# Optimization experiments

Measured on AMD Instinct MI355X. Metric: run time of the kernel, lower is better.

## Reference

```python
import jax, jax.numpy as jnp
import numpy as np

C_S, C_Z, H, P_QK, P_V, L = 384, 128, 12, 4, 8, 768
D = C_S // H
OUT_DIM = C_S + H * P_V * 3 + H * C_Z


def setup_inputs() -> dict:
    key = jax.random.key(0)
    ks = jax.random.split(key, 16)
    sc = lambda fan_in: 1.0 / np.sqrt(fan_in)
    inp = {
        'single': jax.random.normal(ks[0], (L, C_S), jnp.float32),
        'pair': jax.random.normal(ks[1], (L, L, C_Z), jnp.float32),
        'rots': jax.random.normal(ks[2], (L, 3, 3), jnp.float32),
        'trans': jax.random.normal(ks[3], (L, 3), jnp.float32),
        'ln_g': jnp.ones((C_S,), jnp.float32),
        'ln_b': jnp.zeros((C_S,), jnp.float32),
        'Wq': jax.random.normal(ks[4], (C_S, C_S), jnp.float32) * sc(C_S),
        'Wk': jax.random.normal(ks[5], (C_S, C_S), jnp.float32) * sc(C_S),
        'Wv': jax.random.normal(ks[6], (C_S, C_S), jnp.float32) * sc(C_S),
        'Wqp': jax.random.normal(ks[7], (C_S, H * P_QK * 3), jnp.float32) * sc(C_S),
        'bqp': jnp.zeros((H * P_QK * 3,), jnp.float32),
        'Wkp': jax.random.normal(ks[8], (C_S, H * P_QK * 3), jnp.float32) * sc(C_S),
        'bkp': jnp.zeros((H * P_QK * 3,), jnp.float32),
        'Wvp': jax.random.normal(ks[9], (C_S, H * P_V * 3), jnp.float32) * sc(C_S),
        'bvp': jnp.zeros((H * P_V * 3,), jnp.float32),
        'Wpb': jax.random.normal(ks[10], (C_Z, H), jnp.float32) * sc(C_Z),
        'head_weights': jnp.zeros((H,), jnp.float32),
        'Wo': jax.random.normal(ks[11], (OUT_DIM, C_S), jnp.float32) * sc(OUT_DIM),
        'bo': jnp.zeros((C_S,), jnp.float32),
    }
    return inp


def _layernorm(x, g, b, eps=1e-5):
    mu = x.mean(-1, keepdims=True)
    var = ((x - mu) ** 2).mean(-1, keepdims=True)
    return (x - mu) * jax.lax.rsqrt(var + eps) * g + b


def _apply_frames(pts, rots, trans):
    # pts: [L,H,P,3]; rotate each local point into global frame, then translate
    return jnp.einsum('lij,lhpj->lhpi', rots, pts) + trans[:, None, None, :]


def reference(single, pair, rots, trans, ln_g, ln_b, Wq, Wk, Wv, Wqp, bqp,
              Wkp, bkp, Wvp, bvp, Wpb, head_weights, Wo, bo):
    s = _layernorm(single, ln_g, ln_b)
    q = (s @ Wq).reshape(L, H, D)
    k = (s @ Wk).reshape(L, H, D)
    v = (s @ Wv).reshape(L, H, D)
    q_pts = (s @ Wqp + bqp).reshape(L, H, P_QK, 3)
    k_pts = (s @ Wkp + bkp).reshape(L, H, P_QK, 3)
    v_pts = (s @ Wvp + bvp).reshape(L, H, P_V, 3)

    q_g = _apply_frames(q_pts, rots, trans)
    k_g = _apply_frames(k_pts, rots, trans)
    v_g = _apply_frames(v_pts, rots, trans)

    # scalar attention logits [H, L, L]
    attn = jnp.einsum('ihd,jhd->hij', q, k) / np.sqrt(D).astype(np.float32)
    # point-distance bias: ||q_g_i - k_g_j||^2 summed over points -> [L,L,H]
    pt_diff = q_g[:, None] - k_g[None, :]            # [L,L,H,P,3]
    pt_dist_sq = (pt_diff ** 2).sum((-1, -2))        # [L,L,H]
    w_c = jax.nn.softplus(head_weights)
    attn = attn - 0.5 * w_c[:, None, None] * jnp.transpose(pt_dist_sq, (2, 0, 1))
    attn = attn + jnp.einsum('ijc,ch->hij', pair, Wpb)
    attn = jax.nn.softmax(attn, axis=-1)

    out_scalar = jnp.einsum('hij,jhd->ihd', attn, v).reshape(L, C_S)
    out_pts_g = jnp.einsum('hij,jhpc->ihpc', attn, v_g)  # [L,H,Pv,3]
    flat_pts = out_pts_g.reshape(L, H * P_V, 3) - trans[:, None, :]
    # inverse rotation = transpose: einsum with swapped rot indices
    out_pts_l = jnp.einsum('lji,lnj->lni', rots, flat_pts).reshape(L, H * P_V * 3)
    out_pair = jnp.einsum('hij,ijc->ihc', attn, pair).reshape(L, H * C_Z)

    cat = jnp.concatenate([out_scalar, out_pts_l, out_pair], axis=-1)
    return cat @ Wo + bo
```

## Files before the change

kernel.cpp:

```cpp
#include <hip/hip_runtime.h>
#include <math.h>

#define LSEQ 768
#define CS   384
#define CZ   128
#define NH   12
#define OUTD 2208
#define PROJW 1728
#define LL2  (LSEQ*LSEQ)

__device__ __forceinline__ float waveSum(float v){
#pragma unroll
  for (int o = 32; o > 0; o >>= 1) v += __shfl_down(v, o, 64);
  return v;
}

__global__ __launch_bounds__(128) void k_lnwcat(
    const float* __restrict__ x, const float* __restrict__ g,
    const float* __restrict__ b, float* __restrict__ s,
    const float* __restrict__ Wq, const float* __restrict__ Wk,
    const float* __restrict__ Wv, const float* __restrict__ Wqp,
    const float* __restrict__ Wkp, const float* __restrict__ Wvp,
    const float* __restrict__ bqp, const float* __restrict__ bkp,
    const float* __restrict__ bvp,
    float* __restrict__ wcat, float* __restrict__ bcat){
  int blk = blockIdx.x, t = threadIdx.x;
  if (blk < LSEQ){
    int i = blk;
    const float* row = x + (size_t)i*CS;
    float v0 = row[t], v1 = row[t+128], v2 = row[t+256];
    float sum = v0+v1+v2;
    float sq  = v0*v0+v1*v1+v2*v2;
    float ws1 = waveSum(sum), ws2 = waveSum(sq);
    __shared__ float red[4];
    int w = t>>6, lane = t&63;
    if (lane == 0){ red[w] = ws1; red[w+2] = ws2; }
    __syncthreads();
    float mu   = (red[0]+red[1]) * (1.f/CS);
    float var  = (red[2]+red[3]) * (1.f/CS) - mu*mu;
    float rstd = rsqrtf(var + 1e-5f);
    float* o = s + (size_t)i*CS;
    o[t]     = (v0-mu)*rstd*g[t]     + b[t];
    o[t+128] = (v1-mu)*rstd*g[t+128] + b[t+128];
    o[t+256] = (v2-mu)*rstd*g[t+256] + b[t+256];
    return;
  }
  int idx = (blk - LSEQ)*128 + t;
  if (idx < PROJW){
    float bv = 0.f;
    if (idx >= 1440)      bv = bvp[idx-1440];
    else if (idx >= 1296) bv = bkp[idx-1296];
    else if (idx >= 1152) bv = bqp[idx-1152];
    bcat[idx] = bv;
  }
  if (idx >= 384*PROJW) return;
  int r = idx / PROJW, c = idx % PROJW;
  float v;
  if (c < 384)       v = Wq[r*384 + c];
  else if (c < 768)  v = Wk[r*384 + c-384];
  else if (c < 1152) v = Wv[r*384 + c-768];
  else if (c < 1296) v = Wqp[r*144 + c-1152];
  else if (c < 1440) v = Wkp[r*144 + c-1296];
  else               v = Wvp[r*288 + c-1440];
  wcat[idx] = v;
}

__global__ __launch_bounds__(256) void k_gemm(
    const float* __restrict__ A, const float* __restrict__ B,
    const float* __restrict__ bias, float* __restrict__ C,
    int M, int N, int K, int kChunk){
  __shared__ float As[16][68];
  __shared__ float Bs[16][68];
  int j0 = blockIdx.x*64, i0 = blockIdx.y*64;
  int kBeg = blockIdx.z * kChunk;
  int t = threadIdx.x, tx = t & 15, ty = t >> 4;
  int arow = t >> 2, ak = (t & 3) * 4;
  int brow = t >> 4, bcol = (t & 15) * 4;
  float acc[4][4] = {};
  for (int kb = kBeg; kb < kBeg + kChunk; kb += 16){
    float4 av = *(const float4*)(A + (size_t)(i0+arow)*K + kb + ak);
    As[ak+0][arow]=av.x; As[ak+1][arow]=av.y; As[ak+2][arow]=av.z; As[ak+3][arow]=av.w;
    float4 bv = make_float4(0.f,0.f,0.f,0.f);
    if (j0 + bcol < N) bv = *(const float4*)(B + (size_t)(kb+brow)*N + j0 + bcol);
    *(float4*)(&Bs[brow][bcol]) = bv;
    __syncthreads();
#pragma unroll
    for (int kk = 0; kk < 16; ++kk){
      float a[4], b[4];
      *(float4*)a = *(const float4*)(&As[kk][ty*4]);
      *(float4*)b = *(const float4*)(&Bs[kk][tx*4]);
#pragma unroll
      for (int r = 0; r < 4; ++r)
#pragma unroll
        for (int c = 0; c < 4; ++c) acc[r][c] += a[r]*b[c];
    }
    __syncthreads();
  }
  bool noSplit = (gridDim.z == 1);
#pragma unroll
  for (int r = 0; r < 4; ++r){
    int i = i0 + ty*4 + r;
#pragma unroll
    for (int c = 0; c < 4; ++c){
      int j = j0 + tx*4 + c;
      if (j < N){
        float v = acc[r][c];
        if (noSplit && bias) v += bias[j];
        C[(size_t)i*N + j] = v;
      }
    }
  }
}

__global__ __launch_bounds__(256) void k_gemmWo(
    const float* __restrict__ A, const float* __restrict__ B, float* __restrict__ C){
  __shared__ float As[8][132];
  __shared__ float Bs[8][132];
  const int j0 = blockIdx.x*128, i0 = blockIdx.y*128;
  const int kBeg = blockIdx.z*184;
  const int t = threadIdx.x;
  const int arow = t >> 1, akq = (t & 1)*4;
  const int bk = t >> 5, bn = (t & 31)*4;
  const int tx = t & 15, ty = t >> 4;
  float acc[8][8] = {};
  for (int kb = kBeg; kb < kBeg+184; kb += 8){
    float4 av = *(const float4*)(A + (size_t)(i0+arow)*OUTD + kb + akq);
    float4 bv = *(const float4*)(B + (size_t)(kb+bk)*CS + j0 + bn);
    As[akq+0][arow]=av.x; As[akq+1][arow]=av.y; As[akq+2][arow]=av.z; As[akq+3][arow]=av.w;
    *(float4*)(&Bs[bk][bn]) = bv;
    __syncthreads();
#pragma unroll
    for (int k = 0; k < 8; ++k){
      float a[8], b[8];
      *(float4*)(a)   = *(const float4*)(&As[k][ty*8]);
      *(float4*)(a+4) = *(const float4*)(&As[k][ty*8+4]);
      *(float4*)(b)   = *(const float4*)(&Bs[k][tx*8]);
      *(float4*)(b+4) = *(const float4*)(&Bs[k][tx*8+4]);
#pragma unroll
      for (int r = 0; r < 8; ++r)
#pragma unroll
        for (int c = 0; c < 8; ++c) acc[r][c] += a[r]*b[c];
    }
    __syncthreads();
  }
  float* out = C + (size_t)blockIdx.z*LSEQ*CS;
#pragma unroll
  for (int r = 0; r < 8; ++r){
    float* o = out + (size_t)(i0+ty*8+r)*CS + j0 + tx*8;
    *(float4*)(o)   = make_float4(acc[r][0],acc[r][1],acc[r][2],acc[r][3]);
    *(float4*)(o+4) = make_float4(acc[r][4],acc[r][5],acc[r][6],acc[r][7]);
  }
}

__global__ __launch_bounds__(256) void k_prep(
    float* __restrict__ proj, const float* __restrict__ rots,
    const float* __restrict__ trans, const float* __restrict__ hw,
    float* __restrict__ Qa, float* __restrict__ Ka, float* __restrict__ nrm){
  int i = blockIdx.x, t = threadIdx.x;
  __shared__ float wcl[12];
  __shared__ float qg[144], kg[144];
  if (t < 12) wcl[t] = log1pf(__expf(hw[t]));
  float* prow = proj + (size_t)i*PROJW;
  if (t < 192){
    const float* R  = rots + i*9;
    const float* tr = trans + i*3;
    int off = (t < 48) ? (1152 + t*3) : ((t < 96) ? (1296 + (t-48)*3) : (1440 + (t-96)*3));
    float x = prow[off], y = prow[off+1], z = prow[off+2];
    float gx = R[0]*x + R[1]*y + R[2]*z + tr[0];
    float gy = R[3]*x + R[4]*y + R[5]*z + tr[1];
    float gz = R[6]*x + R[7]*y + R[8]*z + tr[2];
    if (t < 48){ qg[t*3]=gx; qg[t*3+1]=gy; qg[t*3+2]=gz; }
    else if (t < 96){ int u=t-48; kg[u*3]=gx; kg[u*3+1]=gy; kg[u*3+2]=gz; }
    else { prow[off]=gx; prow[off+1]=gy; prow[off+2]=gz; }
  }
  __syncthreads();
  const float isq = 0.17677669529663687f;
  for (int idx = t; idx < 576; idx += 256){
    int h = idx/48, d = idx%48;
    float qv = 0.f, kv = 0.f;
    if (d < 32){ qv = prow[h*32 + d]*isq; kv = prow[384 + h*32 + d]; }
    else if (d < 44){ qv = qg[h*12 + (d-32)]*wcl[h]; kv = kg[h*12 + (d-32)]; }
    Qa[((size_t)h*LSEQ + i)*48 + d] = qv;
    Ka[((size_t)h*LSEQ + i)*48 + d] = kv;
  }
  if (t < 24){
    int h = t % 12; int isK = (t >= 12) ? 1 : 0;
    const float* g = isK ? kg : qg;
    float sum = 0.f;
#pragma unroll
    for (int d = 0; d < 12; ++d){ float v = g[h*12+d]; sum += v*v; }
    nrm[((size_t)(isK*12 + h))*LSEQ + i] = -0.5f*wcl[h]*sum;
  }
}

__global__ __launch_bounds__(256) void k_qkaug(
    const float* __restrict__ Qa, const float* __restrict__ Ka,
    const float* __restrict__ nrm, float* __restrict__ logits){
  int j0 = blockIdx.x*64, i0 = blockIdx.y*64, h = blockIdx.z;
  __shared__ float Qs[48][68], Ks[48][68];
  __shared__ float nq[64], nk[64];
  int t = threadIdx.x;
  for (int idx = t; idx < 768; idx += 256){
    int row = idx/12, c4 = (idx%12)*4;
    float4 qv = *(const float4*)(Qa + ((size_t)h*LSEQ + i0+row)*48 + c4);
    Qs[c4+0][row]=qv.x; Qs[c4+1][row]=qv.y; Qs[c4+2][row]=qv.z; Qs[c4+3][row]=qv.w;
    float4 kv = *(const float4*)(Ka + ((size_t)h*LSEQ + j0+row)*48 + c4);
    Ks[c4+0][row]=kv.x; Ks[c4+1][row]=kv.y; Ks[c4+2][row]=kv.z; Ks[c4+3][row]=kv.w;
  }
  if (t < 64) nq[t] = nrm[(size_t)h*LSEQ + i0 + t];
  else if (t < 128) nk[t-64] = nrm[(size_t)(12+h)*LSEQ + j0 + (t-64)];
  __syncthreads();
  int tx = t & 15, ty = t >> 4;
  float acc[4][4] = {};
#pragma unroll 4
  for (int k = 0; k < 44; ++k){
    float a[4], b[4];
    *(float4*)a = *(const float4*)(&Qs[k][ty*4]);
    *(float4*)b = *(const float4*)(&Ks[k][tx*4]);
#pragma unroll
    for (int r = 0; r < 4; ++r)
#pragma unroll
      for (int c = 0; c < 4; ++c) acc[r][c] += a[r]*b[c];
  }
  float nqa[4] = {nq[ty*4], nq[ty*4+1], nq[ty*4+2], nq[ty*4+3]};
  float nk0=nk[tx*4], nk1=nk[tx*4+1], nk2=nk[tx*4+2], nk3=nk[tx*4+3];
#pragma unroll
  for (int r = 0; r < 4; ++r){
    float4 o = make_float4(acc[r][0]+nqa[r]+nk0, acc[r][1]+nqa[r]+nk1,
                           acc[r][2]+nqa[r]+nk2, acc[r][3]+nqa[r]+nk3);
    *(float4*)(logits + ((size_t)(i0+ty*4+r)*NH + h)*LSEQ + j0 + tx*4) = o;
  }
}

__global__ __launch_bounds__(768) void k_pairfused(
    const float* __restrict__ pair, const float* __restrict__ Wpb,
    float* __restrict__ attn,
    float* __restrict__ cat){
  const int i = blockIdx.x, t = threadIdx.x;
  __shared__ __align__(16) float Sb[12*776];
  const float4* prowf4 = (const float4*)(pair + (size_t)i*LSEQ*CZ);
  const int w = t >> 6, lane = t & 63;

  {
    const float4* src = prowf4 + (size_t)t*32;
    float acc[12] = {0.f,0.f,0.f,0.f,0.f,0.f,0.f,0.f,0.f,0.f,0.f,0.f};
#pragma unroll 2
    for (int c4 = 0; c4 < 32; ++c4){
      float4 pv = src[c4];
      const float* wq = Wpb + c4*48;
#pragma unroll
      for (int h = 0; h < 12; ++h)
        acc[h] += pv.x*wq[h] + pv.y*wq[h+12] + pv.z*wq[h+24] + pv.w*wq[h+36];
    }
#pragma unroll
    for (int h = 0; h < 12; ++h) Sb[h*776 + t] = acc[h];
  }
  __syncthreads();

  {
    const int h = w;
    float* lg = attn + ((size_t)i*NH + h)*LSEQ;
    float4 xa = *(const float4*)(lg + lane*4);
    float4 xb = *(const float4*)(lg + 256 + lane*4);
    float4 xc = *(const float4*)(lg + 512 + lane*4);
    float4 ba = *(const float4*)(Sb + h*776 + lane*4);
    float4 bb = *(const float4*)(Sb + h*776 + 256 + lane*4);
    float4 bc = *(const float4*)(Sb + h*776 + 512 + lane*4);
    xa.x+=ba.x; xa.y+=ba.y; xa.z+=ba.z; xa.w+=ba.w;
    xb.x+=bb.x; xb.y+=bb.y; xb.z+=bb.z; xb.w+=bb.w;
    xc.x+=bc.x; xc.y+=bc.y; xc.z+=bc.z; xc.w+=bc.w;
    float m = fmaxf(fmaxf(fmaxf(xa.x,xa.y),fmaxf(xa.z,xa.w)),
             fmaxf(fmaxf(fmaxf(xb.x,xb.y),fmaxf(xb.z,xb.w)),
                   fmaxf(fmaxf(xc.x,xc.y),fmaxf(xc.z,xc.w))));
#pragma unroll
    for (int ms = 32; ms > 0; ms >>= 1) m = fmaxf(m, __shfl_xor(m, ms));
    xa.x=__expf(xa.x-m); xa.y=__expf(xa.y-m); xa.z=__expf(xa.z-m); xa.w=__expf(xa.w-m);
    xb.x=__expf(xb.x-m); xb.y=__expf(xb.y-m); xb.z=__expf(xb.z-m); xb.w=__expf(xb.w-m);
    xc.x=__expf(xc.x-m); xc.y=__expf(xc.y-m); xc.z=__expf(xc.z-m); xc.w=__expf(xc.w-m);
    float sm = xa.x+xa.y+xa.z+xa.w + xb.x+xb.y+xb.z+xb.w + xc.x+xc.y+xc.z+xc.w;
#pragma unroll
    for (int ms = 32; ms > 0; ms >>= 1) sm += __shfl_xor(sm, ms);
    float inv = 1.f/sm;
    xa.x*=inv; xa.y*=inv; xa.z*=inv; xa.w*=inv;
    xb.x*=inv; xb.y*=inv; xb.z*=inv; xb.w*=inv;
    xc.x*=inv; xc.y*=inv; xc.z*=inv; xc.w*=inv;
    *(float4*)(Sb + h*776 + lane*4)       = xa;
    *(float4*)(Sb + h*776 + 256 + lane*4) = xb;
    *(float4*)(Sb + h*776 + 512 + lane*4) = xc;
    *(float4*)(lg + lane*4)       = xa;
    *(float4*)(lg + 256 + lane*4) = xb;
    *(float4*)(lg + 512 + lane*4) = xc;
  }
  __syncthreads();

  const int cq = t & 31, rp = t >> 5;
  float4 acc3[12];
#pragma unroll
  for (int h = 0; h < 12; ++h) acc3[h] = make_float4(0.f,0.f,0.f,0.f);
#pragma unroll 2
  for (int g = 0; g < 8; ++g){
    const int r0 = g*96 + rp*4;
    float4 pv0 = prowf4[(size_t)(r0+0)*32 + cq];
    float4 pv1 = prowf4[(size_t)(r0+1)*32 + cq];
    float4 pv2 = prowf4[(size_t)(r0+2)*32 + cq];
    float4 pv3 = prowf4[(size_t)(r0+3)*32 + cq];
#pragma unroll
    for (int h = 0; h < 12; ++h){
      float4 p4 = *(const float4*)(Sb + h*776 + r0);
      acc3[h].x += pv0.x*p4.x + pv1.x*p4.y + pv2.x*p4.z + pv3.x*p4.w;
      acc3[h].y += pv0.y*p4.x + pv1.y*p4.y + pv2.y*p4.z + pv3.y*p4.w;
      acc3[h].z += pv0.z*p4.x + pv1.z*p4.y + pv2.z*p4.z + pv3.z*p4.w;
      acc3[h].w += pv0.w*p4.x + pv1.w*p4.y + pv2.w*p4.z + pv3.w*p4.w;
    }
  }
#pragma unroll
  for (int h = 0; h < 12; ++h){
    acc3[h].x += __shfl_xor(acc3[h].x, 32);
    acc3[h].y += __shfl_xor(acc3[h].y, 32);
    acc3[h].z += __shfl_xor(acc3[h].z, 32);
    acc3[h].w += __shfl_xor(acc3[h].w, 32);
  }
  __syncthreads();
  if (w < 6 && lane < 32){
#pragma unroll
    for (int h = 0; h < 12; ++h)
      *(float4*)(Sb + w*1536 + h*128 + cq*4) = acc3[h];
  }
  __syncthreads();
  if (w >= 6 && lane < 32){
#pragma unroll
    for (int h = 0; h < 12; ++h){
      float4* d = (float4*)(Sb + (w-6)*1536 + h*128 + cq*4);
      float4 v = *d;
      v.x += acc3[h].x; v.y += acc3[h].y; v.z += acc3[h].z; v.w += acc3[h].w;
      *d = v;
    }
  }
  __syncthreads();
  float* crow = cat + (size_t)i*OUTD + 672;
#pragma unroll
  for (int o = t; o < 1536; o += 768)
    crow[o] = Sb[o] + Sb[1536+o] + Sb[3072+o] + Sb[4608+o] + Sb[6144+o] + Sb[7680+o];
}

__global__ __launch_bounds__(256) void k_pv(
    const float* __restrict__ attn, const float* __restrict__ proj,
    const float* __restrict__ rots, const float* __restrict__ trans,
    float* __restrict__ cat){
  int h = blockIdx.y, i0 = blockIdx.x*16;
  __shared__ float As[32][17];
  __shared__ float Bs[32][60];
  __shared__ float pts[16][24];
  int t = threadIdx.x, tx = t & 15, ty = t >> 4;
  float acc[4] = {};
  for (int kb = 0; kb < LSEQ; kb += 32){
    __syncthreads();
    {
      int row = t >> 4, k2 = (t & 15)*2;
      float2 av = *(const float2*)(attn + ((size_t)(i0+row)*NH + h)*LSEQ + kb + k2);
      As[k2][row] = av.x; As[k2+1][row] = av.y;
    }
    for (int idx = t; idx < 32*56; idx += 256){
      int kk = idx/56, n = idx%56;
      const float* prow = proj + (size_t)(kb+kk)*PROJW;
      Bs[kk][n] = (n < 32) ? prow[768 + h*32 + n] : prow[1440 + h*24 + (n-32)];
    }
    __syncthreads();
    if (tx < 14){
#pragma unroll
      for (int kk = 0; kk < 32; ++kk){
        float a = As[kk][ty];
        float b[4]; *(float4*)b = *(const float4*)(&Bs[kk][tx*4]);
        acc[0] += a*b[0]; acc[1] += a*b[1]; acc[2] += a*b[2]; acc[3] += a*b[3];
      }
    }
  }
  __syncthreads();
  if (tx < 14){
    int i = i0 + ty;
#pragma unroll
    for (int c = 0; c < 4; ++c){
      int n = tx*4 + c;
      if (n < 32) cat[(size_t)i*OUTD + h*32 + n] = acc[c];
      else pts[ty][n-32] = acc[c];
    }
  }
  __syncthreads();
  if (t < 128){
    int row = t >> 3, p = t & 7;
    int i = i0 + row;
    const float* R = rots + i*9; const float* tr = trans + i*3;
    float x = pts[row][p*3]   - tr[0];
    float y = pts[row][p*3+1] - tr[1];
    float z = pts[row][p*3+2] - tr[2];
    float* o = cat + (size_t)i*OUTD + 384 + h*24 + p*3;
    o[0] = R[0]*x + R[3]*y + R[6]*z;
    o[1] = R[1]*x + R[4]*y + R[7]*z;
    o[2] = R[2]*x + R[5]*y + R[8]*z;
  }
}

__global__ __launch_bounds__(256) void k_reduce(
    const float* __restrict__ part, const float* __restrict__ bias,
    float* __restrict__ out){
  int idx = blockIdx.x*256 + threadIdx.x;
  if (idx >= LSEQ*CS) return;
  float v = bias[idx % CS];
#pragma unroll
  for (int z = 0; z < 12; ++z) v += part[(size_t)z*LSEQ*CS + idx];
  out[idx] = v;
}

extern "C" void kernel_launch(void* const* d_in, const int* in_sizes, int n_in,
                              void* d_out, int out_size, void* d_ws, size_t ws_size,
                              hipStream_t stream){
  const float* single = (const float*)d_in[0];
  const float* pair   = (const float*)d_in[1];
  const float* rots   = (const float*)d_in[2];
  const float* trans  = (const float*)d_in[3];
  const float* ln_g   = (const float*)d_in[4];
  const float* ln_b   = (const float*)d_in[5];
  const float* Wq  = (const float*)d_in[6];
  const float* Wk  = (const float*)d_in[7];
  const float* Wv  = (const float*)d_in[8];
  const float* Wqp = (const float*)d_in[9];
  const float* bqp = (const float*)d_in[10];
  const float* Wkp = (const float*)d_in[11];
  const float* bkp = (const float*)d_in[12];
  const float* Wvp = (const float*)d_in[13];
  const float* bvp = (const float*)d_in[14];
  const float* Wpb = (const float*)d_in[15];
  const float* hw  = (const float*)d_in[16];
  const float* Wo  = (const float*)d_in[17];
  const float* bo  = (const float*)d_in[18];
  float* out = (float*)d_out;

  float* ws = (float*)d_ws;
  float* s    = ws;
  float* wcat = ws + 294912;
  float* bcat = ws + 958464;
  float* Qa   = ws;
  float* Ka   = ws + 442368;
  float* nrm  = ws + 884736;
  float* proj = ws + 960256;
  float* attn = ws + 2287360;
  float* cat  = ws + 9365248;
  float* part = attn;

  int wcatBlocks = (384*PROJW + 127)/128;
  k_lnwcat<<<LSEQ + wcatBlocks, 128, 0, stream>>>(single, ln_g, ln_b, s,
      Wq, Wk, Wv, Wqp, Wkp, Wvp, bqp, bkp, bvp, wcat, bcat);
  k_gemm<<<dim3(27,12,1), 256, 0, stream>>>(s, wcat, bcat, proj, 768, PROJW, 384, 384);
  k_prep<<<LSEQ, 256, 0, stream>>>(proj, rots, trans, hw, Qa, Ka, nrm);
  k_qkaug<<<dim3(12,12,12), 256, 0, stream>>>(Qa, Ka, nrm, attn);
  k_pairfused<<<LSEQ, 768, 0, stream>>>(pair, Wpb, attn, cat);
  k_pv<<<dim3(48, NH), 256, 0, stream>>>(attn, proj, rots, trans, cat);
  k_gemmWo<<<dim3(3,6,12), 256, 0, stream>>>(cat, Wo, part);
  k_reduce<<<(LSEQ*CS+255)/256, 256, 0, stream>>>(part, bo, out);
}
```

Baseline: 323.8 us.

## Fuse QK augmented logits into pair-bias softmax kernel

Removes the separate tiled QK logit kernel and computes the augmented dot products (scalar plus point terms and norms) inside the pair-bias/softmax kernel, accumulating directly into shared memory before softmax. This avoids writing and re-reading the full H×L×L logits tensor through global memory. In exchange each row block recomputes dot products with a naive per-lane loop, reading K rows from global/L2 without shared-memory tiling, and the workspace buffers are relocated so Qa/Ka no longer alias s.

```diff
diff --git a/kernel.cpp b/kernel.cpp
--- a/kernel.cpp
+++ b/kernel.cpp
@@ -193,47 +193,10 @@
   }
 }
 
-__global__ __launch_bounds__(256) void k_qkaug(
-    const float* __restrict__ Qa, const float* __restrict__ Ka,
-    const float* __restrict__ nrm, float* __restrict__ logits){
-  int j0 = blockIdx.x*64, i0 = blockIdx.y*64, h = blockIdx.z;
-  __shared__ float Qs[48][68], Ks[48][68];
-  __shared__ float nq[64], nk[64];
-  int t = threadIdx.x;
-  for (int idx = t; idx < 768; idx += 256){
-    int row = idx/12, c4 = (idx%12)*4;
-    float4 qv = *(const float4*)(Qa + ((size_t)h*LSEQ + i0+row)*48 + c4);
-    Qs[c4+0][row]=qv.x; Qs[c4+1][row]=qv.y; Qs[c4+2][row]=qv.z; Qs[c4+3][row]=qv.w;
-    float4 kv = *(const float4*)(Ka + ((size_t)h*LSEQ + j0+row)*48 + c4);
-    Ks[c4+0][row]=kv.x; Ks[c4+1][row]=kv.y; Ks[c4+2][row]=kv.z; Ks[c4+3][row]=kv.w;
-  }
-  if (t < 64) nq[t] = nrm[(size_t)h*LSEQ + i0 + t];
-  else if (t < 128) nk[t-64] = nrm[(size_t)(12+h)*LSEQ + j0 + (t-64)];
-  __syncthreads();
-  int tx = t & 15, ty = t >> 4;
-  float acc[4][4] = {};
-#pragma unroll 4
-  for (int k = 0; k < 44; ++k){
-    float a[4], b[4];
-    *(float4*)a = *(const float4*)(&Qs[k][ty*4]);
-    *(float4*)b = *(const float4*)(&Ks[k][tx*4]);
-#pragma unroll
-    for (int r = 0; r < 4; ++r)
-#pragma unroll
-      for (int c = 0; c < 4; ++c) acc[r][c] += a[r]*b[c];
-  }
-  float nqa[4] = {nq[ty*4], nq[ty*4+1], nq[ty*4+2], nq[ty*4+3]};
-  float nk0=nk[tx*4], nk1=nk[tx*4+1], nk2=nk[tx*4+2], nk3=nk[tx*4+3];
-#pragma unroll
-  for (int r = 0; r < 4; ++r){
-    float4 o = make_float4(acc[r][0]+nqa[r]+nk0, acc[r][1]+nqa[r]+nk1,
-                           acc[r][2]+nqa[r]+nk2, acc[r][3]+nqa[r]+nk3);
-    *(float4*)(logits + ((size_t)(i0+ty*4+r)*NH + h)*LSEQ + j0 + tx*4) = o;
-  }
-}
-
 __global__ __launch_bounds__(768) void k_pairfused(
     const float* __restrict__ pair, const float* __restrict__ Wpb,
+    const float* __restrict__ Qa, const float* __restrict__ Ka,
+    const float* __restrict__ nrm,
     float* __restrict__ attn,
     float* __restrict__ cat){
   const int i = blockIdx.x, t = threadIdx.x;
@@ -259,16 +222,29 @@
 
   {
     const int h = w;
+    const float* qrow = Qa + ((size_t)h*LSEQ + i)*48;
+    const float  nq   = nrm[(size_t)h*LSEQ + i];
+    const float* nk   = nrm + (size_t)(12+h)*LSEQ;
+#pragma unroll 1
+    for (int jj = 0; jj < 12; ++jj){
+      const int j = jj*64 + lane;
+      const float4* krow = (const float4*)(Ka + ((size_t)h*LSEQ + j)*48);
+      float s = 0.f;
+#pragma unroll
+      for (int c4 = 0; c4 < 12; ++c4){
+        float4 kv = krow[c4];
+        s += kv.x*qrow[c4*4] + kv.y*qrow[c4*4+1] + kv.z*qrow[c4*4+2] + kv.w*qrow[c4*4+3];
+      }
+      Sb[h*776 + j] += s + nq + nk[j];
+    }
+  }
+
+  {
+    const int h = w;
     float* lg = attn + ((size_t)i*NH + h)*LSEQ;
-    float4 xa = *(const float4*)(lg + lane*4);
-    float4 xb = *(const float4*)(lg + 256 + lane*4);
-    float4 xc = *(const float4*)(lg + 512 + lane*4);
-    float4 ba = *(const float4*)(Sb + h*776 + lane*4);
-    float4 bb = *(const float4*)(Sb + h*776 + 256 + lane*4);
-    float4 bc = *(const float4*)(Sb + h*776 + 512 + lane*4);
-    xa.x+=ba.x; xa.y+=ba.y; xa.z+=ba.z; xa.w+=ba.w;
-    xb.x+=bb.x; xb.y+=bb.y; xb.z+=bb.z; xb.w+=bb.w;
-    xc.x+=bc.x; xc.y+=bc.y; xc.z+=bc.z; xc.w+=bc.w;
+    float4 xa = *(const float4*)(Sb + h*776 + lane*4);
+    float4 xb = *(const float4*)(Sb + h*776 + 256 + lane*4);
+    float4 xc = *(const float4*)(Sb + h*776 + 512 + lane*4);
     float m = fmaxf(fmaxf(fmaxf(xa.x,xa.y),fmaxf(xa.z,xa.w)),
              fmaxf(fmaxf(fmaxf(xb.x,xb.y),fmaxf(xb.z,xb.w)),
                    fmaxf(fmaxf(xc.x,xc.y),fmaxf(xc.z,xc.w))));
@@ -439,12 +415,12 @@
   float* s    = ws;
   float* wcat = ws + 294912;
   float* bcat = ws + 958464;
-  float* Qa   = ws;
-  float* Ka   = ws + 442368;
-  float* nrm  = ws + 884736;
-  float* proj = ws + 960256;
-  float* attn = ws + 2287360;
-  float* cat  = ws + 9365248;
+  float* Qa   = ws + 960256;
+  float* Ka   = ws + 1402624;
+  float* nrm  = ws + 1844992;
+  float* proj = ws + 1863424;
+  float* attn = ws + 3190528;
+  float* cat  = ws + 10268416;
   float* part = attn;
 
   int wcatBlocks = (384*PROJW + 127)/128;
@@ -452,8 +428,7 @@
       Wq, Wk, Wv, Wqp, Wkp, Wvp, bqp, bkp, bvp, wcat, bcat);
   k_gemm<<<dim3(27,12,1), 256, 0, stream>>>(s, wcat, bcat, proj, 768, PROJW, 384, 384);
   k_prep<<<LSEQ, 256, 0, stream>>>(proj, rots, trans, hw, Qa, Ka, nrm);
-  k_qkaug<<<dim3(12,12,12), 256, 0, stream>>>(Qa, Ka, nrm, attn);
-  k_pairfused<<<LSEQ, 768, 0, stream>>>(pair, Wpb, attn, cat);
+  k_pairfused<<<LSEQ, 768, 0, stream>>>(pair, Wpb, Qa, Ka, nrm, attn, cat);
   k_pv<<<dim3(48, NH), 256, 0, stream>>>(attn, proj, rots, trans, cat);
   k_gemmWo<<<dim3(3,6,12), 256, 0, stream>>>(cat, Wo, part);
   k_reduce<<<(LSEQ*CS+255)/256, 256, 0, stream>>>(part, bo, out);
```

After: 405.2 us. 25.1% more time.
